# Kernel optimization log

Measured on AMD Instinct MI355X. Metric: run time of the kernel, lower is better.

Reference implementation:

```python
import jax, jax.numpy as jnp
import numpy as np

B, S, HID = 2, 2048, 2048
H, G = 32, 8            # query heads, kv heads
D = HID // H            # head_dim = 64
QPG = H // G            # q heads per kv group = 4


def setup_inputs() -> dict:
    key = jax.random.key(0)
    ks = jax.random.split(key, 5)
    sc = 0.02
    return {
        "x": jax.random.normal(ks[0], (B, S, HID), jnp.float32),
        "Wq": jax.random.normal(ks[1], (HID, HID), jnp.float32) * sc,
        "bq": jnp.zeros((HID,), jnp.float32),
        "Wk": jax.random.normal(ks[2], (HID, G * D), jnp.float32) * sc,
        "bk": jnp.zeros((G * D,), jnp.float32),
        "Wv": jax.random.normal(ks[3], (HID, G * D), jnp.float32) * sc,
        "bv": jnp.zeros((G * D,), jnp.float32),
        "Wo": jax.random.normal(ks[4], (HID, HID), jnp.float32) * sc,
        "bo": jnp.zeros((HID,), jnp.float32),
    }


def reference(x, Wq, bq, Wk, bk, Wv, bv, Wo, bo):
    b, s, _ = x.shape
    # projections (weights stored as [in, out])
    q = (x @ Wq + bq).reshape(b, s, G, QPG, D)      # [b,s,g,p,d]
    k = (x @ Wk + bk).reshape(b, s, G, D)           # [b,s,g,d]
    v = (x @ Wv + bv).reshape(b, s, G, D)
    scale = 1.0 / jnp.sqrt(jnp.asarray(D, x.dtype))
    # grouped attention: repeat_interleave of K/V expressed as shared g axis
    scores = jnp.einsum('bsgpd,btgd->bgpst', q, k) * scale  # [b,g,p,s,t]
    w = jax.nn.softmax(scores, axis=-1)
    o = jnp.einsum('bgpst,btgd->bsgpd', w, v)               # [b,s,g,p,d]
    o = o.reshape(b, s, HID)
    return o @ Wo + bo
```

## Files before the change

### kernel.cpp

```cpp
#include <hip/hip_runtime.h>
#include <hip/hip_bf16.h>


typedef __attribute__((ext_vector_type(8))) short shortx8;
typedef __attribute__((ext_vector_type(4))) float floatx4;

#define SEQ 2048
#define QSC 0.1803368801111204f

#if __has_builtin(__builtin_amdgcn_exp2f)
#define EXP2F(x) __builtin_amdgcn_exp2f(x)
#else
#define EXP2F(x) __expf((x) * 0.6931471805599453f)
#endif

__device__ __forceinline__ unsigned short f2bf(float f) {
  union { float f; unsigned u; } a; a.f = f;
  unsigned u = a.u;
  u += 0x7fffu + ((u >> 16) & 1u);
  return (unsigned short)(u >> 16);
}
__device__ __forceinline__ unsigned pk2f(float lo, float hi) {
  union { float f; unsigned u; } a, b; a.f = lo; b.f = hi;
  return ((a.u + 0x8000u) >> 16) | (((b.u + 0x8000u) >> 16) << 16);
}

__device__ __forceinline__ void gload16(const unsigned short* g, unsigned short* l) {
  __builtin_amdgcn_global_load_lds((const __attribute__((address_space(1))) void*)g,
                                   (__attribute__((address_space(3))) void*)l, 16, 0, 0);
}

__global__ void prep_kernel(const float* __restrict__ x,
                            const float* __restrict__ Wq, const float* __restrict__ Wk,
                            const float* __restrict__ Wv, const float* __restrict__ Wo,
                            const float* __restrict__ bq, const float* __restrict__ bk,
                            const float* __restrict__ bv,
                            unsigned short* __restrict__ WT,
                            unsigned short* __restrict__ WoT,
                            unsigned short* __restrict__ xb,
                            float* __restrict__ bqkv) {
  const int z = blockIdx.z;
  if (z == 4) {
    int fb = blockIdx.y * 64 + blockIdx.x;
    int tid = threadIdx.y * 32 + threadIdx.x;
    int i = fb * 2048 + tid * 8;
    float4 v0 = *(const float4*)(x + i);
    float4 v1 = *(const float4*)(x + i + 4);
    ushort4 o0, o1;
    o0.x = f2bf(v0.x); o0.y = f2bf(v0.y); o0.z = f2bf(v0.z); o0.w = f2bf(v0.w);
    o1.x = f2bf(v1.x); o1.y = f2bf(v1.y); o1.z = f2bf(v1.z); o1.w = f2bf(v1.w);
    *(ushort4*)(xb + i) = o0;
    *(ushort4*)(xb + i + 4) = o1;
    return;
  }
  if (z == 5) {
    int fb = blockIdx.y * 64 + blockIdx.x;
    if (fb >= 12) return;
    int i = fb * 256 + threadIdx.y * 32 + threadIdx.x;
    if (i < 2048) bqkv[i] = bq[i] * QSC;
    else if (i < 2560) bqkv[i] = bk[i - 2048];
    else if (i < 3072) bqkv[i] = bv[i - 2560];
    return;
  }
  const float* W; unsigned short* D; int N; float sc = 1.f;
  if (z == 0)      { W = Wq; D = WT;               N = 2048; sc = QSC; }
  else if (z == 1) { W = Wk; D = WT + 2048 * 2048; N = 512; }
  else if (z == 2) { W = Wv; D = WT + 2560 * 2048; N = 512; }
  else             { W = Wo; D = WoT;              N = 2048; }
  if (blockIdx.x * 32 >= N) return;

  __shared__ float tile[32][33];
  int xx = blockIdx.x * 32 + threadIdx.x;
  int y0 = blockIdx.y * 32;
  for (int i = 0; i < 32; i += 8)
    tile[threadIdx.y + i][threadIdx.x] = W[(size_t)(y0 + threadIdx.y + i) * N + xx];
  __syncthreads();
  int nx = y0 + threadIdx.x;
  int ny = blockIdx.x * 32 + threadIdx.y;
  for (int i = 0; i < 32; i += 8)
    D[(size_t)(ny + i) * 2048 + nx] = f2bf(tile[threadIdx.x][threadIdx.y + i] * sc);
}

template <int MODE>
__global__ __launch_bounds__(256) void gemm_bt(const unsigned short* __restrict__ A,
                                               const unsigned short* __restrict__ BT,
                                               const float* __restrict__ bias,
                                               void* __restrict__ Cout,
                                               unsigned short* __restrict__ Kbuf,
                                               unsigned short* __restrict__ Vt,
                                               int M, int N, int K) {
  __shared__ __align__(16) unsigned short As[128 * 64];
  __shared__ __align__(16) unsigned short Bs[128 * 64];
  const int m0 = blockIdx.x * 128, n0 = blockIdx.y * 128;
  const int tid = threadIdx.x;
  const int lane = tid & 63, wave = tid >> 6;
  const int l15 = lane & 15, quad = lane >> 4;
  const int wm = (wave & 1) * 64, wn = (wave >> 1) * 64;

  const int r8 = lane >> 3;
  const int clog = (lane & 7) ^ r8;
  const unsigned short* aSrc = A + (size_t)(m0 + wave * 32 + r8) * K + clog * 8;
  const unsigned short* bSrc = BT + (size_t)(n0 + wave * 32 + r8) * K + clog * 8;
  unsigned short* aDst = &As[wave * 2048];
  unsigned short* bDst = &Bs[wave * 2048];

  const int s = l15 & 7;
  int aoff[4], boff[4];
#pragma unroll
  for (int i = 0; i < 4; i++) aoff[i] = (wm + i * 16 + l15) * 64 + (quad ^ s) * 8;
#pragma unroll
  for (int j = 0; j < 4; j++) boff[j] = (wn + j * 16 + l15) * 64 + (quad ^ s) * 8;

  floatx4 acc[4][4];
#pragma unroll
  for (int i = 0; i < 4; i++)
#pragma unroll
    for (int j = 0; j < 4; j++)
#pragma unroll
      for (int r = 0; r < 4; r++) acc[i][j][r] = 0.f;

  for (int k0 = 0; k0 < K; k0 += 64) {
    __syncthreads();
#pragma unroll
    for (int j = 0; j < 4; j++) {
      gload16(aSrc + (size_t)j * 8 * K + k0, aDst + j * 512);
      gload16(bSrc + (size_t)j * 8 * K + k0, bDst + j * 512);
    }
    __syncthreads();
    {
      shortx8 af[4], bf[4];
#pragma unroll
      for (int i = 0; i < 4; i++) af[i] = *(const shortx8*)&As[aoff[i]];
#pragma unroll
      for (int j = 0; j < 4; j++) bf[j] = *(const shortx8*)&Bs[boff[j]];
#pragma unroll
      for (int i = 0; i < 4; i++)
#pragma unroll
        for (int j = 0; j < 4; j++)
          acc[i][j] = __builtin_amdgcn_mfma_f32_16x16x32_bf16(af[i], bf[j], acc[i][j], 0, 0, 0);
#pragma unroll
      for (int i = 0; i < 4; i++) af[i] = *(const shortx8*)&As[aoff[i] ^ 32];
#pragma unroll
      for (int j = 0; j < 4; j++) bf[j] = *(const shortx8*)&Bs[boff[j] ^ 32];
#pragma unroll
      for (int i = 0; i < 4; i++)
#pragma unroll
        for (int j = 0; j < 4; j++)
          acc[i][j] = __builtin_amdgcn_mfma_f32_16x16x32_bf16(af[i], bf[j], acc[i][j], 0, 0, 0);
    }
  }

#pragma unroll
  for (int i = 0; i < 4; i++) {
#pragma unroll
    for (int j = 0; j < 4; j++) {
      int col = n0 + wn + j * 16 + l15;
      float bv = bias[col];
#pragma unroll
      for (int r = 0; r < 4; r++) {
        int row = m0 + wm + i * 16 + quad * 4 + r;
        float v = acc[i][j][r] + bv;
        if (MODE == 0) {
          ((float*)Cout)[(size_t)row * N + col] = v;
        } else {
          if (col < 2048) {
            ((unsigned short*)Cout)[(size_t)row * 2048 + col] = f2bf(v);
          } else if (col < 2560) {
            Kbuf[(size_t)row * 512 + (col - 2048)] = f2bf(v);
          } else {
            int g = (col - 2560) >> 6, d = (col - 2560) & 63;
            int b = row >> 11, sidx = row & 2047;
            Vt[(size_t)(((g << 1) | b) * 64 + d) * 2048 + sidx] = f2bf(v);
          }
        }
      }
    }
  }
}

__global__ __launch_bounds__(256, 3) void attn_kernel(const unsigned short* __restrict__ Qb,
                                                      const unsigned short* __restrict__ Kb,
                                                      const unsigned short* __restrict__ Vt,
                                                      unsigned short* __restrict__ O) {
  const int qt = blockIdx.x, g = blockIdx.y, b = blockIdx.z;
  const int tid = threadIdx.x;
  const int lane = tid & 63, wave = tid >> 6;
  const int h = g * 4 + wave;
  const int l15 = lane & 15, quad = lane >> 4;

  __shared__ __align__(16) unsigned short Ks[2][64 * 64];
  __shared__ __align__(16) unsigned short Vs[2][64 * 64];
  __shared__ __align__(16) unsigned short Ps[4 * 2048];

  shortx8 qf[2][2];
  {
    const unsigned short* qp = Qb + (size_t)(b * SEQ + qt * 32 + l15) * 2048 + h * 64 + quad * 8;
#pragma unroll
    for (int a = 0; a < 2; a++) {
      qf[a][0] = *(const shortx8*)(qp + (size_t)a * 16 * 2048);
      qf[a][1] = *(const shortx8*)(qp + (size_t)a * 16 * 2048 + 32);
    }
  }

  const int r8 = lane >> 3;
  const int clog = (lane & 7) ^ r8;
  const unsigned short* kSrc = Kb + ((size_t)b * SEQ + wave * 16 + r8) * 512 + g * 64 + clog * 8;
  const unsigned short* vSrc = Vt + ((size_t)((g * 2 + b) * 64 + wave * 16 + r8)) * 2048 + clog * 8;

  const int s = l15 & 7;
  int foff[4];
#pragma unroll
  for (int i = 0; i < 4; i++) foff[i] = (i * 16 + l15) * 64 + ((quad ^ s) * 8);

  const int pbase = wave * 2048 + l15 * 64;
  int pw[4];
#pragma unroll
  for (int i = 0; i < 4; i++) pw[i] = (((i * 2 + (quad >> 1)) ^ s) * 8) + (quad & 1) * 4;
  int pr[2];
#pragma unroll
  for (int ks = 0; ks < 2; ks++) pr[ks] = ((ks * 4 + quad) ^ s) * 8;

  shortx8 ones;
#pragma unroll
  for (int j = 0; j < 8; j++) ones[j] = (short)0x3F80;

  floatx4 oacc[2][4], lacc[2];
#pragma unroll
  for (int a = 0; a < 2; a++) {
#pragma unroll
    for (int r = 0; r < 4; r++) lacc[a][r] = 0.f;
#pragma unroll
    for (int nd = 0; nd < 4; nd++)
#pragma unroll
      for (int r = 0; r < 4; r++) oacc[a][nd][r] = 0.f;
  }

  {
    unsigned short* kD = &Ks[0][wave * 1024];
    unsigned short* vD = &Vs[0][wave * 1024];
    gload16(kSrc, kD);
    gload16(kSrc + (size_t)8 * 512, kD + 512);
    gload16(vSrc, vD);
    gload16(vSrc + (size_t)8 * 2048, vD + 512);
  }
  __syncthreads();

  for (int it = 0; it < SEQ / 64; it++) {
    const int p = it & 1;
    if (it < SEQ / 64 - 1) {
      const size_t t1 = (size_t)(it + 1) * 64;
      unsigned short* kD = &Ks[p ^ 1][wave * 1024];
      unsigned short* vD = &Vs[p ^ 1][wave * 1024];
      gload16(kSrc + t1 * 512, kD);
      gload16(kSrc + (t1 + 8) * 512, kD + 512);
      gload16(vSrc + t1, vD);
      gload16(vSrc + (size_t)8 * 2048 + t1, vD + 512);
    }

    shortx8 kf[4][2];
#pragma unroll
    for (int i = 0; i < 4; i++) {
      kf[i][0] = *(const shortx8*)&Ks[p][foff[i]];
      kf[i][1] = *(const shortx8*)&Ks[p][foff[i] ^ 32];
    }

#pragma unroll
    for (int a = 0; a < 2; a++) {
      floatx4 sc[4];
      __builtin_amdgcn_s_setprio(1);
#pragma unroll
      for (int i = 0; i < 4; i++) {
        floatx4 c = {0.f, 0.f, 0.f, 0.f};
        c = __builtin_amdgcn_mfma_f32_16x16x32_bf16(kf[i][0], qf[a][0], c, 0, 0, 0);
        c = __builtin_amdgcn_mfma_f32_16x16x32_bf16(kf[i][1], qf[a][1], c, 0, 0, 0);
        sc[i] = c;
      }
      __builtin_amdgcn_s_setprio(0);
#pragma unroll
      for (int i = 0; i < 4; i++) {
        float p0 = EXP2F(sc[i][0]), p1 = EXP2F(sc[i][1]);
        float p2 = EXP2F(sc[i][2]), p3 = EXP2F(sc[i][3]);
        uint2 w; w.x = pk2f(p0, p1); w.y = pk2f(p2, p3);
        *(uint2*)&Ps[pbase + a * 1024 + pw[i]] = w;
      }
    }

    shortx8 vf[4][2];
#pragma unroll
    for (int nd = 0; nd < 4; nd++) {
      vf[nd][0] = *(const shortx8*)&Vs[p][foff[nd]];
      vf[nd][1] = *(const shortx8*)&Vs[p][foff[nd] ^ 32];
    }
#pragma unroll
    for (int a = 0; a < 2; a++) {
#pragma unroll
      for (int ks = 0; ks < 2; ks++) {
        shortx8 pf = *(const shortx8*)&Ps[pbase + a * 1024 + pr[ks]];
        __builtin_amdgcn_s_setprio(1);
#pragma unroll
        for (int nd = 0; nd < 4; nd++)
          oacc[a][nd] = __builtin_amdgcn_mfma_f32_16x16x32_bf16(vf[nd][ks], pf, oacc[a][nd], 0, 0, 0);
        lacc[a] = __builtin_amdgcn_mfma_f32_16x16x32_bf16(ones, pf, lacc[a], 0, 0, 0);
        __builtin_amdgcn_s_setprio(0);
      }
    }
    __syncthreads();
  }

#pragma unroll
  for (int a = 0; a < 2; a++) {
    float inv = 1.f / lacc[a][0];
    unsigned short* oPtr = O + (size_t)(b * SEQ + qt * 32 + a * 16 + l15) * 2048 + h * 64 + quad * 4;
#pragma unroll
    for (int nd = 0; nd < 4; nd++) {
      uint2 w;
      w.x = (unsigned)f2bf(oacc[a][nd][0] * inv) | ((unsigned)f2bf(oacc[a][nd][1] * inv) << 16);
      w.y = (unsigned)f2bf(oacc[a][nd][2] * inv) | ((unsigned)f2bf(oacc[a][nd][3] * inv) << 16);
      *(uint2*)(oPtr + nd * 16) = w;
    }
  }
}

extern "C" void kernel_launch(void* const* d_in, const int* in_sizes, int n_in,
                              void* d_out, int out_size, void* d_ws, size_t ws_size,
                              hipStream_t stream) {
  const float* x  = (const float*)d_in[0];
  const float* Wq = (const float*)d_in[1];
  const float* bq = (const float*)d_in[2];
  const float* Wk = (const float*)d_in[3];
  const float* bk = (const float*)d_in[4];
  const float* Wv = (const float*)d_in[5];
  const float* bv = (const float*)d_in[6];
  const float* Wo = (const float*)d_in[7];
  const float* bo = (const float*)d_in[8];
  float* out = (float*)d_out;

  char* ws = (char*)d_ws;
  unsigned short* WTall = (unsigned short*)ws;
  unsigned short* WoT   = (unsigned short*)(ws + 12582912);
  float*          bqkv  = (float*)(ws + 20971520);
  unsigned short* xb    = (unsigned short*)(ws + 20987904);
  unsigned short* Qbuf  = (unsigned short*)(ws + 37765120);
  unsigned short* Kbuf  = (unsigned short*)(ws + 54542336);
  unsigned short* Vt    = (unsigned short*)(ws + 58736640);
  unsigned short* Og    = xb;

  prep_kernel<<<dim3(64, 64, 6), dim3(32, 8), 0, stream>>>(
      x, Wq, Wk, Wv, Wo, bq, bk, bv, WTall, WoT, xb, bqkv);

  gemm_bt<2><<<dim3(32, 24), 256, 0, stream>>>(xb, WTall, bqkv, Qbuf, Kbuf, Vt, 4096, 3072, 2048);

  attn_kernel<<<dim3(64, 8, 2), 256, 0, stream>>>(Qbuf, Kbuf, Vt, Og);

  gemm_bt<0><<<dim3(32, 16), 256, 0, stream>>>(Og, WoT, bo, out, nullptr, nullptr, 4096, 2048, 2048);
}
```

Baseline: 339.5 us.

## Transpose softmax probabilities in registers via permlane swap instead of LDS

Removes the per-wave LDS staging buffer for the P matrix. The exp'd scores are rearranged into the MFMA B-operand layout with v_permlane32_swap and ds_swizzle plus selects. This avoids LDS stores and loads for P and cuts LDS use by 16KB per block, and the launch bound is raised from 3 to 4 blocks per CU to use that. In exchange it adds cross-lane ops and selects, and the higher occupancy target caps the register budget more tightly, which could cause spills.

```diff
diff --git a/kernel.cpp b/kernel.cpp
--- a/kernel.cpp
+++ b/kernel.cpp
@@ -23,6 +23,10 @@
 __device__ __forceinline__ unsigned pk2f(float lo, float hi) {
   union { float f; unsigned u; } a, b; a.f = lo; b.f = hi;
   return ((a.u + 0x8000u) >> 16) | (((b.u + 0x8000u) >> 16) << 16);
+}
+
+__device__ __forceinline__ void plswap(unsigned &a, unsigned &b) {
+  asm("v_permlane32_swap_b32 %0, %1" : "+v"(a), "+v"(b));
 }
 
 __device__ __forceinline__ void gload16(const unsigned short* g, unsigned short* l) {
@@ -178,7 +182,7 @@
   }
 }
 
-__global__ __launch_bounds__(256, 3) void attn_kernel(const unsigned short* __restrict__ Qb,
+__global__ __launch_bounds__(256, 4) void attn_kernel(const unsigned short* __restrict__ Qb,
                                                       const unsigned short* __restrict__ Kb,
                                                       const unsigned short* __restrict__ Vt,
                                                       unsigned short* __restrict__ O) {
@@ -190,7 +194,6 @@
 
   __shared__ __align__(16) unsigned short Ks[2][64 * 64];
   __shared__ __align__(16) unsigned short Vs[2][64 * 64];
-  __shared__ __align__(16) unsigned short Ps[4 * 2048];
 
   shortx8 qf[2][2];
   {
@@ -212,13 +215,7 @@
 #pragma unroll
   for (int i = 0; i < 4; i++) foff[i] = (i * 16 + l15) * 64 + ((quad ^ s) * 8);
 
-  const int pbase = wave * 2048 + l15 * 64;
-  int pw[4];
-#pragma unroll
-  for (int i = 0; i < 4; i++) pw[i] = (((i * 2 + (quad >> 1)) ^ s) * 8) + (quad & 1) * 4;
-  int pr[2];
-#pragma unroll
-  for (int ks = 0; ks < 2; ks++) pr[ks] = ((ks * 4 + quad) ^ s) * 8;
+  const bool hb4 = (quad & 1) != 0;
 
   shortx8 ones;
 #pragma unroll
@@ -264,6 +261,7 @@
       kf[i][1] = *(const shortx8*)&Ks[p][foff[i] ^ 32];
     }
 
+    shortx8 pfr[2][2];
 #pragma unroll
     for (int a = 0; a < 2; a++) {
       floatx4 sc[4];
@@ -276,13 +274,33 @@
         sc[i] = c;
       }
       __builtin_amdgcn_s_setprio(0);
-#pragma unroll
-      for (int i = 0; i < 4; i++) {
-        float p0 = EXP2F(sc[i][0]), p1 = EXP2F(sc[i][1]);
-        float p2 = EXP2F(sc[i][2]), p3 = EXP2F(sc[i][3]);
-        uint2 w; w.x = pk2f(p0, p1); w.y = pk2f(p2, p3);
-        *(uint2*)&Ps[pbase + a * 1024 + pw[i]] = w;
-      }
+      unsigned e0a = pk2f(EXP2F(sc[0][0]), EXP2F(sc[0][1]));
+      unsigned e0b = pk2f(EXP2F(sc[0][2]), EXP2F(sc[0][3]));
+      unsigned e1a = pk2f(EXP2F(sc[1][0]), EXP2F(sc[1][1]));
+      unsigned e1b = pk2f(EXP2F(sc[1][2]), EXP2F(sc[1][3]));
+      unsigned e2a = pk2f(EXP2F(sc[2][0]), EXP2F(sc[2][1]));
+      unsigned e2b = pk2f(EXP2F(sc[2][2]), EXP2F(sc[2][3]));
+      unsigned e3a = pk2f(EXP2F(sc[3][0]), EXP2F(sc[3][1]));
+      unsigned e3b = pk2f(EXP2F(sc[3][2]), EXP2F(sc[3][3]));
+      plswap(e0a, e1a);
+      plswap(e0b, e1b);
+      plswap(e2a, e3a);
+      plswap(e2b, e3b);
+      unsigned x0 = hb4 ? e0a : e1a;
+      unsigned y0 = hb4 ? e0b : e1b;
+      unsigned x1 = hb4 ? e2a : e3a;
+      unsigned y1 = hb4 ? e2b : e3b;
+      x0 = (unsigned)__builtin_amdgcn_ds_swizzle((int)x0, 0x401F);
+      y0 = (unsigned)__builtin_amdgcn_ds_swizzle((int)y0, 0x401F);
+      x1 = (unsigned)__builtin_amdgcn_ds_swizzle((int)x1, 0x401F);
+      y1 = (unsigned)__builtin_amdgcn_ds_swizzle((int)y1, 0x401F);
+      union { unsigned u[4]; shortx8 v; } P0, P1;
+      P0.u[0] = hb4 ? x0 : e0a;  P0.u[1] = hb4 ? y0 : e0b;
+      P0.u[2] = hb4 ? e1a : x0;  P0.u[3] = hb4 ? e1b : y0;
+      P1.u[0] = hb4 ? x1 : e2a;  P1.u[1] = hb4 ? y1 : e2b;
+      P1.u[2] = hb4 ? e3a : x1;  P1.u[3] = hb4 ? e3b : y1;
+      pfr[a][0] = P0.v;
+      pfr[a][1] = P1.v;
     }
 
     shortx8 vf[4][2];
@@ -295,7 +313,7 @@
     for (int a = 0; a < 2; a++) {
 #pragma unroll
       for (int ks = 0; ks < 2; ks++) {
-        shortx8 pf = *(const shortx8*)&Ps[pbase + a * 1024 + pr[ks]];
+        shortx8 pf = pfr[a][ks];
         __builtin_amdgcn_s_setprio(1);
 #pragma unroll
         for (int nd = 0; nd < 4; nd++)
```

Measured after the change: 322.8 us. 4.9% less time.

## Keep attention probabilities in registers via permlane swaps instead of LDS

Applied to the files above, without the earlier changes.

Removes the LDS staging buffer for the softmax probabilities. The exp results are packed with the hardware bf16 convert instruction and rearranged into the PV MFMA operand layout using permlane32/permlane16 swaps. This eliminates the LDS write/read round trip and frees 16KB of shared memory, which is why the occupancy hint rises from 3 to 4 blocks. The risks are that the register permutation must exactly match the old LDS layout, and the higher occupancy target may cause register pressure or spills.

```diff
diff --git a/kernel.cpp b/kernel.cpp
--- a/kernel.cpp
+++ b/kernel.cpp
@@ -20,9 +20,18 @@
   u += 0x7fffu + ((u >> 16) & 1u);
   return (unsigned short)(u >> 16);
 }
-__device__ __forceinline__ unsigned pk2f(float lo, float hi) {
-  union { float f; unsigned u; } a, b; a.f = lo; b.f = hi;
-  return ((a.u + 0x8000u) >> 16) | (((b.u + 0x8000u) >> 16) << 16);
+
+__device__ __forceinline__ unsigned cvtpkbf(float lo, float hi) {
+  unsigned r;
+  asm("v_cvt_pk_bf16_f32 %0, %1, %2" : "=v"(r) : "v"(lo), "v"(hi));
+  return r;
+}
+
+__device__ __forceinline__ void plswap(unsigned &a, unsigned &b) {
+  asm("v_permlane32_swap_b32 %0, %1" : "+v"(a), "+v"(b));
+}
+__device__ __forceinline__ void pl16swap(unsigned &a, unsigned &b) {
+  asm("v_permlane16_swap_b32 %0, %1" : "+v"(a), "+v"(b));
 }
 
 __device__ __forceinline__ void gload16(const unsigned short* g, unsigned short* l) {
@@ -178,7 +187,7 @@
   }
 }
 
-__global__ __launch_bounds__(256, 3) void attn_kernel(const unsigned short* __restrict__ Qb,
+__global__ __launch_bounds__(256, 4) void attn_kernel(const unsigned short* __restrict__ Qb,
                                                       const unsigned short* __restrict__ Kb,
                                                       const unsigned short* __restrict__ Vt,
                                                       unsigned short* __restrict__ O) {
@@ -190,7 +199,6 @@
 
   __shared__ __align__(16) unsigned short Ks[2][64 * 64];
   __shared__ __align__(16) unsigned short Vs[2][64 * 64];
-  __shared__ __align__(16) unsigned short Ps[4 * 2048];
 
   shortx8 qf[2][2];
   {
@@ -211,14 +219,6 @@
   int foff[4];
 #pragma unroll
   for (int i = 0; i < 4; i++) foff[i] = (i * 16 + l15) * 64 + ((quad ^ s) * 8);
-
-  const int pbase = wave * 2048 + l15 * 64;
-  int pw[4];
-#pragma unroll
-  for (int i = 0; i < 4; i++) pw[i] = (((i * 2 + (quad >> 1)) ^ s) * 8) + (quad & 1) * 4;
-  int pr[2];
-#pragma unroll
-  for (int ks = 0; ks < 2; ks++) pr[ks] = ((ks * 4 + quad) ^ s) * 8;
 
   shortx8 ones;
 #pragma unroll
@@ -264,6 +264,7 @@
       kf[i][1] = *(const shortx8*)&Ks[p][foff[i] ^ 32];
     }
 
+    shortx8 pfr[2][2];
 #pragma unroll
     for (int a = 0; a < 2; a++) {
       floatx4 sc[4];
@@ -276,13 +277,23 @@
         sc[i] = c;
       }
       __builtin_amdgcn_s_setprio(0);
-#pragma unroll
-      for (int i = 0; i < 4; i++) {
-        float p0 = EXP2F(sc[i][0]), p1 = EXP2F(sc[i][1]);
-        float p2 = EXP2F(sc[i][2]), p3 = EXP2F(sc[i][3]);
-        uint2 w; w.x = pk2f(p0, p1); w.y = pk2f(p2, p3);
-        *(uint2*)&Ps[pbase + a * 1024 + pw[i]] = w;
-      }
+      unsigned E00 = cvtpkbf(EXP2F(sc[0][0]), EXP2F(sc[0][1]));
+      unsigned E01 = cvtpkbf(EXP2F(sc[0][2]), EXP2F(sc[0][3]));
+      unsigned E10 = cvtpkbf(EXP2F(sc[1][0]), EXP2F(sc[1][1]));
+      unsigned E11 = cvtpkbf(EXP2F(sc[1][2]), EXP2F(sc[1][3]));
+      unsigned E20 = cvtpkbf(EXP2F(sc[2][0]), EXP2F(sc[2][1]));
+      unsigned E21 = cvtpkbf(EXP2F(sc[2][2]), EXP2F(sc[2][3]));
+      unsigned E30 = cvtpkbf(EXP2F(sc[3][0]), EXP2F(sc[3][1]));
+      unsigned E31 = cvtpkbf(EXP2F(sc[3][2]), EXP2F(sc[3][3]));
+      plswap(E00, E10); plswap(E01, E11);
+      plswap(E20, E30); plswap(E21, E31);
+      pl16swap(E00, E10); pl16swap(E01, E11);
+      pl16swap(E20, E30); pl16swap(E21, E31);
+      union { unsigned u[4]; shortx8 v; } P0, P1;
+      P0.u[0] = E00; P0.u[1] = E01; P0.u[2] = E10; P0.u[3] = E11;
+      P1.u[0] = E20; P1.u[1] = E21; P1.u[2] = E30; P1.u[3] = E31;
+      pfr[a][0] = P0.v;
+      pfr[a][1] = P1.v;
     }
 
     shortx8 vf[4][2];
@@ -295,7 +306,7 @@
     for (int a = 0; a < 2; a++) {
 #pragma unroll
       for (int ks = 0; ks < 2; ks++) {
-        shortx8 pf = *(const shortx8*)&Ps[pbase + a * 1024 + pr[ks]];
+        shortx8 pf = pfr[a][ks];
         __builtin_amdgcn_s_setprio(1);
 #pragma unroll
         for (int nd = 0; nd < 4; nd++)
```

Result: faster. 304.8 us (-10.2%).
